# Optimization experiments

Hardware: AMD Instinct MI355X
Metric: run time of the kernel (lower is better)

The kernel has to match this reference:

```python
import jax, jax.numpy as jnp
import numpy as np
from jax.experimental import sparse as jsparse

N_ITEMS = 20000   # item catalog size (S is [N_ITEMS, N_ITEMS])
N_USERS = 2048    # user batch
NNZ = 4_000_000


def setup_inputs() -> dict:
    key = jax.random.key(0)
    k1, k2, k3, k4 = jax.random.split(key, 4)
    X = jax.random.normal(k1, (N_USERS, N_ITEMS), dtype=jnp.float32)
    S_vals = jax.random.normal(k2, (NNZ,), dtype=jnp.float32)
    S_rows = jax.random.randint(k3, (NNZ,), 0, N_ITEMS, dtype=jnp.int32)
    S_cols = jax.random.randint(k4, (NNZ,), 0, N_ITEMS, dtype=jnp.int32)
    return {"X": X, "S_vals": S_vals, "S_rows": S_rows, "S_cols": S_cols}


def reference(X, S_vals, S_rows, S_cols):
    # torch.sparse.mm(S, X.t()).t()  ==  X @ S^T, with S sparse COO.
    indices = jnp.stack([S_rows, S_cols], axis=1)  # [nnz, 2]
    S = jsparse.BCOO((S_vals, indices), shape=(N_ITEMS, N_ITEMS))
    # (S @ X^T)^T -> [n_users, n_items]; duplicate indices sum, matching COO semantics.
    return (S @ X.T).T
```

## Files before the change

### kernel.cpp

```cpp
#include <hip/hip_runtime.h>

#define N_ITEMS 20000
#define N_USERS 2048
#define NNZ     4000000
#define LDP     2112

typedef float f32x4 __attribute__((ext_vector_type(4)));

#define OFF_XT      ((size_t)0)
#define OFF_CSRPK   ((size_t)84480000)
#define OFF_ROWPTR  (OFF_CSRPK + 16000000)
#define OFF_CURSOR  (OFF_ROWPTR + 80128)
#define OFF_CNT     (OFF_CURSOR + 80128)
#define OFF_BSUM    (OFF_CNT + 80128)

static __device__ __forceinline__ unsigned short f2bf(float f) {
  unsigned u = __float_as_uint(f);
  unsigned r = (u + 0x7fffu + ((u >> 16) & 1u)) >> 16;
  return (unsigned short)r;
}

__global__ __launch_bounds__(256) void transpose_kernel(
    const float* __restrict__ X, unsigned short* __restrict__ XT) {
  __shared__ float tile[64][65];
  int k0 = blockIdx.x * 64;
  int u0 = blockIdx.y * 64;
  int lane = threadIdx.x & 63;
  int dq = threadIdx.x >> 6;
  #pragma unroll
  for (int m = 0; m < 16; ++m) {
    int u = u0 + dq + 4 * m;
    int k = k0 + lane;
    float v = 0.f;
    if (k < N_ITEMS) v = X[(size_t)u * N_ITEMS + k];
    tile[lane][dq + 4 * m] = v;
  }
  __syncthreads();
  #pragma unroll
  for (int m = 0; m < 16; ++m) {
    int k = k0 + dq + 4 * m;
    if (k < N_ITEMS)
      XT[(size_t)k * LDP + u0 + lane] = f2bf(tile[dq + 4 * m][lane]);
  }
}

__global__ void zero_kernel(int* __restrict__ p, int n) {
  int i = blockIdx.x * blockDim.x + threadIdx.x;
  if (i < n) p[i] = 0;
}

__global__ void count_kernel(const int* __restrict__ rows, int* __restrict__ cnt) {
  int i = blockIdx.x * blockDim.x + threadIdx.x;
  if (i < NNZ) atomicAdd(&cnt[rows[i]], 1);
}

__global__ __launch_bounds__(1024) void scan1_kernel(
    const int* __restrict__ cnt, int* __restrict__ loc, int* __restrict__ bsum) {
  __shared__ int buf[1024];
  int tid = threadIdx.x;
  int i = blockIdx.x * 1024 + tid;
  int x = (i < N_ITEMS) ? cnt[i] : 0;
  buf[tid] = x;
  __syncthreads();
  for (int off = 1; off < 1024; off <<= 1) {
    int y = (tid >= off) ? buf[tid - off] : 0;
    __syncthreads();
    buf[tid] += y;
    __syncthreads();
  }
  if (i < N_ITEMS) loc[i] = buf[tid] - x;
  if (tid == 1023) bsum[blockIdx.x] = buf[1023];
}

__global__ void scan2_kernel(int* __restrict__ bsum, int nblk) {
  if (threadIdx.x == 0) {
    int s = 0;
    for (int b = 0; b < nblk; ++b) { int t = bsum[b]; bsum[b] = s; s += t; }
  }
}

__global__ __launch_bounds__(1024) void scan3_kernel(
    int* __restrict__ row_ptr, const int* __restrict__ bsum, int* __restrict__ cursor) {
  int i = blockIdx.x * 1024 + threadIdx.x;
  if (i < N_ITEMS) {
    int v = row_ptr[i] + bsum[blockIdx.x];
    row_ptr[i] = v;
    cursor[i] = v;
  }
  if (i == 0) row_ptr[N_ITEMS] = NNZ;
}

__global__ void scatter_kernel(const int* __restrict__ rows, const int* __restrict__ cols,
                               const float* __restrict__ vals, int* __restrict__ cursor,
                               unsigned* __restrict__ csr_pk) {
  int i = blockIdx.x * blockDim.x + threadIdx.x;
  if (i < NNZ) {
    int r = rows[i];
    int pos = atomicAdd(&cursor[r], 1);
    csr_pk[pos] = (unsigned)cols[i] | ((unsigned)f2bf(vals[i]) << 16);
  }
}

__global__ __launch_bounds__(256) void spmm_kernel(
    const int* __restrict__ row_ptr, const unsigned* __restrict__ csr_pk,
    const unsigned short* __restrict__ xt, float* __restrict__ out) {
  __shared__ float tile[16][132];
  int wg = blockIdx.x;
  int xcd = wg & 7;
  int slot = wg >> 3;
  int combo = slot / 1250;
  int rb = slot - combo * 1250;
  int uchunk = xcd * 2 + combo;
  int u0 = uchunk * 128;
  int r0 = rb * 16;
  int lane = threadIdx.x & 63;
  int wave = __builtin_amdgcn_readfirstlane((int)(threadIdx.x >> 6));
  const unsigned short* xt_u = xt + u0 + 2 * lane;

#define PROC8(E)                                                         \
  {                                                                      \
    unsigned x2[8];                                                      \
    _Pragma("unroll")                                                    \
    for (int k = 0; k < 8; ++k)                                          \
      x2[k] = *reinterpret_cast<const unsigned*>(xt_u + (E[k] & 0x7fffu) * LDP); \
    _Pragma("unroll")                                                    \
    for (int k = 0; k < 8; ++k) {                                        \
      float v  = __uint_as_float(E[k] & 0xffff0000u);                    \
      float xl = __uint_as_float(x2[k] << 16);                           \
      float xh = __uint_as_float(x2[k] & 0xffff0000u);                   \
      if (k & 1) { a2 = fmaf(v, xl, a2); a3 = fmaf(v, xh, a3); }         \
      else       { a0 = fmaf(v, xl, a0); a1 = fmaf(v, xh, a1); }         \
    }                                                                    \
  }

  #pragma unroll
  for (int rr = 0; rr < 4; ++rr) {
    int r = r0 + wave * 4 + rr;
    int jb = __builtin_amdgcn_readfirstlane(row_ptr[r]);
    int je = __builtin_amdgcn_readfirstlane(row_ptr[r + 1]);
    float a0 = 0.f, a1 = 0.f, a2 = 0.f, a3 = 0.f;
    int n8 = (je - jb) >> 3;
    if (n8 > 0) {
      unsigned e[8];
      #pragma unroll
      for (int k = 0; k < 8; ++k) e[k] = csr_pk[jb + k];
      for (int b = 1; b < n8; ++b) {
        unsigned en[8];
        int jn = jb + b * 8;
        #pragma unroll
        for (int k = 0; k < 8; ++k) en[k] = csr_pk[jn + k];
        PROC8(e)
        #pragma unroll
        for (int k = 0; k < 8; ++k) e[k] = en[k];
      }
      PROC8(e)
    }
    for (int j = jb + n8 * 8; j < je; ++j) {
      unsigned ee = csr_pk[j];
      unsigned x2 = *reinterpret_cast<const unsigned*>(xt_u + (ee & 0x7fffu) * LDP);
      float v = __uint_as_float(ee & 0xffff0000u);
      a0 = fmaf(v, __uint_as_float(x2 << 16), a0);
      a1 = fmaf(v, __uint_as_float(x2 & 0xffff0000u), a1);
    }
    tile[wave * 4 + rr][2 * lane]     = a0 + a2;
    tile[wave * 4 + rr][2 * lane + 1] = a1 + a3;
  }
#undef PROC8
  __syncthreads();
  int ul = threadIdx.x >> 1;
  int rseg = (threadIdx.x & 1) * 8;
  float* op = &out[(size_t)(u0 + ul) * N_ITEMS + r0 + rseg];
  f32x4 o0, o1;
  o0.x = tile[rseg + 0][ul]; o0.y = tile[rseg + 1][ul];
  o0.z = tile[rseg + 2][ul]; o0.w = tile[rseg + 3][ul];
  o1.x = tile[rseg + 4][ul]; o1.y = tile[rseg + 5][ul];
  o1.z = tile[rseg + 6][ul]; o1.w = tile[rseg + 7][ul];
  __builtin_nontemporal_store(o0, reinterpret_cast<f32x4*>(op));
  __builtin_nontemporal_store(o1, reinterpret_cast<f32x4*>(op) + 1);
}

extern "C" void kernel_launch(void* const* d_in, const int* in_sizes, int n_in,
                              void* d_out, int out_size, void* d_ws, size_t ws_size,
                              hipStream_t stream) {
  const float* X      = (const float*)d_in[0];
  const float* S_vals = (const float*)d_in[1];
  const int*   S_rows = (const int*)d_in[2];
  const int*   S_cols = (const int*)d_in[3];
  float* out = (float*)d_out;

  char* ws = (char*)d_ws;
  unsigned short* XT  = (unsigned short*)(ws + OFF_XT);
  unsigned* csr_pk    = (unsigned*)(ws + OFF_CSRPK);
  int* row_ptr        = (int*)(ws + OFF_ROWPTR);
  int* cursor         = (int*)(ws + OFF_CURSOR);
  int* cnt            = (int*)(ws + OFF_CNT);
  int* bsum           = (int*)(ws + OFF_BSUM);

  const int nblk = (N_ITEMS + 1023) / 1024;

  transpose_kernel<<<dim3((N_ITEMS + 63) / 64, N_USERS / 64), 256, 0, stream>>>(X, XT);
  zero_kernel<<<(N_ITEMS + 255) / 256, 256, 0, stream>>>(cnt, N_ITEMS);
  count_kernel<<<NNZ / 256, 256, 0, stream>>>(S_rows, cnt);
  scan1_kernel<<<nblk, 1024, 0, stream>>>(cnt, row_ptr, bsum);
  scan2_kernel<<<1, 64, 0, stream>>>(bsum, nblk);
  scan3_kernel<<<nblk, 1024, 0, stream>>>(row_ptr, bsum, cursor);
  scatter_kernel<<<NNZ / 256, 256, 0, stream>>>(S_rows, S_cols, S_vals, cursor, csr_pk);
  spmm_kernel<<<1250 * 16, 256, 0, stream>>>(row_ptr, csr_pk, XT, out);
}
```

Measured before the change: 1.261 ms.

## Split CSR rows by column half to localize XT gathers in SpMM

```diff
diff --git a/kernel.cpp b/kernel.cpp
--- a/kernel.cpp
+++ b/kernel.cpp
@@ -4,15 +4,17 @@
 #define N_USERS 2048
 #define NNZ     4000000
 #define LDP     2112
+#define HALF_ITEMS 10000
+#define NBINS   (2 * N_ITEMS)
 
 typedef float f32x4 __attribute__((ext_vector_type(4)));
 
 #define OFF_XT      ((size_t)0)
 #define OFF_CSRPK   ((size_t)84480000)
 #define OFF_ROWPTR  (OFF_CSRPK + 16000000)
-#define OFF_CURSOR  (OFF_ROWPTR + 80128)
-#define OFF_CNT     (OFF_CURSOR + 80128)
-#define OFF_BSUM    (OFF_CNT + 80128)
+#define OFF_CURSOR  (OFF_ROWPTR + 160256)
+#define OFF_CNT     (OFF_CURSOR + 160256)
+#define OFF_BSUM    (OFF_CNT + 160256)
 
 static __device__ __forceinline__ unsigned short f2bf(float f) {
   unsigned u = __float_as_uint(f);
@@ -44,14 +46,17 @@
   }
 }
 
-__global__ void zero_kernel(int* __restrict__ p, int n) {
-  int i = blockIdx.x * blockDim.x + threadIdx.x;
-  if (i < n) p[i] = 0;
-}
-
-__global__ void count_kernel(const int* __restrict__ rows, int* __restrict__ cnt) {
-  int i = blockIdx.x * blockDim.x + threadIdx.x;
-  if (i < NNZ) atomicAdd(&cnt[rows[i]], 1);
+__global__ void count_kernel(const int* __restrict__ rows, const int* __restrict__ cols,
+                             int* __restrict__ cnt) {
+  int i = (blockIdx.x * blockDim.x + threadIdx.x) * 4;
+  if (i < NNZ) {
+    int4 r4 = *reinterpret_cast<const int4*>(rows + i);
+    int4 c4 = *reinterpret_cast<const int4*>(cols + i);
+    atomicAdd(&cnt[2 * r4.x + (c4.x >= HALF_ITEMS ? 1 : 0)], 1);
+    atomicAdd(&cnt[2 * r4.y + (c4.y >= HALF_ITEMS ? 1 : 0)], 1);
+    atomicAdd(&cnt[2 * r4.z + (c4.z >= HALF_ITEMS ? 1 : 0)], 1);
+    atomicAdd(&cnt[2 * r4.w + (c4.w >= HALF_ITEMS ? 1 : 0)], 1);
+  }
 }
 
 __global__ __launch_bounds__(1024) void scan1_kernel(
@@ -59,7 +64,7 @@
   __shared__ int buf[1024];
   int tid = threadIdx.x;
   int i = blockIdx.x * 1024 + tid;
-  int x = (i < N_ITEMS) ? cnt[i] : 0;
+  int x = (i < NBINS) ? cnt[i] : 0;
   buf[tid] = x;
   __syncthreads();
   for (int off = 1; off < 1024; off <<= 1) {
@@ -68,7 +73,7 @@
     buf[tid] += y;
     __syncthreads();
   }
-  if (i < N_ITEMS) loc[i] = buf[tid] - x;
+  if (i < NBINS) loc[i] = buf[tid] - x;
   if (tid == 1023) bsum[blockIdx.x] = buf[1023];
 }
 
@@ -82,22 +87,31 @@
 __global__ __launch_bounds__(1024) void scan3_kernel(
     int* __restrict__ row_ptr, const int* __restrict__ bsum, int* __restrict__ cursor) {
   int i = blockIdx.x * 1024 + threadIdx.x;
-  if (i < N_ITEMS) {
+  if (i < NBINS) {
     int v = row_ptr[i] + bsum[blockIdx.x];
     row_ptr[i] = v;
     cursor[i] = v;
   }
-  if (i == 0) row_ptr[N_ITEMS] = NNZ;
+  if (i == 0) row_ptr[NBINS] = NNZ;
 }
 
 __global__ void scatter_kernel(const int* __restrict__ rows, const int* __restrict__ cols,
                                const float* __restrict__ vals, int* __restrict__ cursor,
                                unsigned* __restrict__ csr_pk) {
-  int i = blockIdx.x * blockDim.x + threadIdx.x;
+  int i = (blockIdx.x * blockDim.x + threadIdx.x) * 4;
   if (i < NNZ) {
-    int r = rows[i];
-    int pos = atomicAdd(&cursor[r], 1);
-    csr_pk[pos] = (unsigned)cols[i] | ((unsigned)f2bf(vals[i]) << 16);
+    int4   r4 = *reinterpret_cast<const int4*>(rows + i);
+    int4   c4 = *reinterpret_cast<const int4*>(cols + i);
+    float4 v4 = *reinterpret_cast<const float4*>(vals + i);
+    #pragma unroll
+    for (int k = 0; k < 4; ++k) {
+      int c = (k == 0) ? c4.x : (k == 1) ? c4.y : (k == 2) ? c4.z : c4.w;
+      int r = (k == 0) ? r4.x : (k == 1) ? r4.y : (k == 2) ? r4.z : r4.w;
+      float v = (k == 0) ? v4.x : (k == 1) ? v4.y : (k == 2) ? v4.z : v4.w;
+      int h = (c >= HALF_ITEMS) ? 1 : 0;
+      int pos = atomicAdd(&cursor[2 * r + h], 1);
+      csr_pk[pos] = (unsigned)(c - h * HALF_ITEMS) | ((unsigned)f2bf(v) << 16);
+    }
   }
 }
 
@@ -115,14 +129,19 @@
   int r0 = rb * 16;
   int lane = threadIdx.x & 63;
   int wave = __builtin_amdgcn_readfirstlane((int)(threadIdx.x >> 6));
-  const unsigned short* xt_u = xt + u0 + 2 * lane;
+
+  float acc[4][4];
+  #pragma unroll
+  for (int rr = 0; rr < 4; ++rr)
+    #pragma unroll
+    for (int k = 0; k < 4; ++k) acc[rr][k] = 0.f;
 
 #define PROC8(E)                                                         \
   {                                                                      \
     unsigned x2[8];                                                      \
     _Pragma("unroll")                                                    \
     for (int k = 0; k < 8; ++k)                                          \
-      x2[k] = *reinterpret_cast<const unsigned*>(xt_u + (E[k] & 0x7fffu) * LDP); \
+      x2[k] = *reinterpret_cast<const unsigned*>(xt_h + (E[k] & 0x3fffu) * LDP); \
     _Pragma("unroll")                                                    \
     for (int k = 0; k < 8; ++k) {                                        \
       float v  = __uint_as_float(E[k] & 0xffff0000u);                    \
@@ -134,38 +153,47 @@
   }
 
   #pragma unroll
+  for (int h = 0; h < 2; ++h) {
+    const unsigned short* xt_h = xt + (size_t)h * HALF_ITEMS * LDP + u0 + 2 * lane;
+    #pragma unroll
+    for (int rr = 0; rr < 4; ++rr) {
+      int seg = 2 * (r0 + wave * 4 + rr) + h;
+      int jb = __builtin_amdgcn_readfirstlane(row_ptr[seg]);
+      int je = __builtin_amdgcn_readfirstlane(row_ptr[seg + 1]);
+      float a0 = acc[rr][0], a1 = acc[rr][1], a2 = acc[rr][2], a3 = acc[rr][3];
+      int n8 = (je - jb) >> 3;
+      if (n8 > 0) {
+        unsigned e[8];
+        #pragma unroll
+        for (int k = 0; k < 8; ++k) e[k] = csr_pk[jb + k];
+        for (int b = 1; b < n8; ++b) {
+          unsigned en[8];
+          int jn = jb + b * 8;
+          #pragma unroll
+          for (int k = 0; k < 8; ++k) en[k] = csr_pk[jn + k];
+          PROC8(e)
+          #pragma unroll
+          for (int k = 0; k < 8; ++k) e[k] = en[k];
+        }
+        PROC8(e)
+      }
+      for (int j = jb + n8 * 8; j < je; ++j) {
+        unsigned ee = csr_pk[j];
+        unsigned x2 = *reinterpret_cast<const unsigned*>(xt_h + (ee & 0x3fffu) * LDP);
+        float v = __uint_as_float(ee & 0xffff0000u);
+        a0 = fmaf(v, __uint_as_float(x2 << 16), a0);
+        a1 = fmaf(v, __uint_as_float(x2 & 0xffff0000u), a1);
+      }
+      acc[rr][0] = a0; acc[rr][1] = a1; acc[rr][2] = a2; acc[rr][3] = a3;
+    }
+  }
+#undef PROC8
+
+  #pragma unroll
   for (int rr = 0; rr < 4; ++rr) {
-    int r = r0 + wave * 4 + rr;
-    int jb = __builtin_amdgcn_readfirstlane(row_ptr[r]);
-    int je = __builtin_amdgcn_readfirstlane(row_ptr[r + 1]);
-    float a0 = 0.f, a1 = 0.f, a2 = 0.f, a3 = 0.f;
-    int n8 = (je - jb) >> 3;
-    if (n8 > 0) {
-      unsigned e[8];
-      #pragma unroll
-      for (int k = 0; k < 8; ++k) e[k] = csr_pk[jb + k];
-      for (int b = 1; b < n8; ++b) {
-        unsigned en[8];
-        int jn = jb + b * 8;
-        #pragma unroll
-        for (int k = 0; k < 8; ++k) en[k] = csr_pk[jn + k];
-        PROC8(e)
-        #pragma unroll
-        for (int k = 0; k < 8; ++k) e[k] = en[k];
-      }
-      PROC8(e)
-    }
-    for (int j = jb + n8 * 8; j < je; ++j) {
-      unsigned ee = csr_pk[j];
-      unsigned x2 = *reinterpret_cast<const unsigned*>(xt_u + (ee & 0x7fffu) * LDP);
-      float v = __uint_as_float(ee & 0xffff0000u);
-      a0 = fmaf(v, __uint_as_float(x2 << 16), a0);
-      a1 = fmaf(v, __uint_as_float(x2 & 0xffff0000u), a1);
-    }
-    tile[wave * 4 + rr][2 * lane]     = a0 + a2;
-    tile[wave * 4 + rr][2 * lane + 1] = a1 + a3;
-  }
-#undef PROC8
+    tile[wave * 4 + rr][2 * lane]     = acc[rr][0] + acc[rr][2];
+    tile[wave * 4 + rr][2 * lane + 1] = acc[rr][1] + acc[rr][3];
+  }
   __syncthreads();
   int ul = threadIdx.x >> 1;
   int rseg = (threadIdx.x & 1) * 8;
@@ -196,14 +224,15 @@
   int* cnt            = (int*)(ws + OFF_CNT);
   int* bsum           = (int*)(ws + OFF_BSUM);
 
-  const int nblk = (N_ITEMS + 1023) / 1024;
+  const int nblk = (NBINS + 1023) / 1024;
+  const int nq   = (NNZ / 4 + 255) / 256;
 
   transpose_kernel<<<dim3((N_ITEMS + 63) / 64, N_USERS / 64), 256, 0, stream>>>(X, XT);
-  zero_kernel<<<(N_ITEMS + 255) / 256, 256, 0, stream>>>(cnt, N_ITEMS);
-  count_kernel<<<NNZ / 256, 256, 0, stream>>>(S_rows, cnt);
+  hipMemsetAsync(cnt, 0, NBINS * sizeof(int), stream);
+  count_kernel<<<nq, 256, 0, stream>>>(S_rows, S_cols, cnt);
   scan1_kernel<<<nblk, 1024, 0, stream>>>(cnt, row_ptr, bsum);
   scan2_kernel<<<1, 64, 0, stream>>>(bsum, nblk);
   scan3_kernel<<<nblk, 1024, 0, stream>>>(row_ptr, bsum, cursor);
-  scatter_kernel<<<NNZ / 256, 256, 0, stream>>>(S_rows, S_cols, S_vals, cursor, csr_pk);
+  scatter_kernel<<<nq, 256, 0, stream>>>(S_rows, S_cols, S_vals, cursor, csr_pk);
   spmm_kernel<<<1250 * 16, 256, 0, stream>>>(row_ptr, csr_pk, XT, out);
 }
```

After: 1.294 ms. +2.7%, slower.
